# Optimization experiments

Measured on AMD Instinct MI355X. Metric: run time of the kernel, lower is better.

## Reference

```python
import jax, jax.numpy as jnp
import numpy as np

N_MLP = 16
LATENT = 1024
S0, S1, S2, OUT = 512, 256, 128, 3


def _make_grid(n_grid_step):
    # matches np.meshgrid (indexing='xy') then reshape(-1): points (x, y)
    p = np.linspace(-1.0, 1.0, n_grid_step, dtype=np.float32)
    X, Y = np.meshgrid(p, p)
    return jnp.asarray(np.stack([X.ravel(), Y.ravel()], axis=-1))  # [G, 2]


def setup_inputs() -> dict:
    key = jax.random.key(0)
    ks = jax.random.split(key, 12)
    sc = lambda fan_in: 1.0 / np.sqrt(fan_in)
    inp = {
        "x0": jax.random.normal(ks[0], (LATENT,), jnp.float32),
        "W0a": jax.random.normal(ks[1], (N_MLP, S0, LATENT), jnp.float32) * sc(LATENT),
        "b0a": jax.random.normal(ks[2], (N_MLP, S0), jnp.float32) * sc(LATENT),
        "W0b": jax.random.normal(ks[3], (N_MLP, S0, 2), jnp.float32) * sc(2),
        "b0b": jax.random.normal(ks[4], (N_MLP, S0), jnp.float32) * sc(2),
        "W1": jax.random.normal(ks[5], (N_MLP, S1, S0), jnp.float32) * sc(S0),
        "b1": jax.random.normal(ks[6], (N_MLP, S1), jnp.float32) * sc(S0),
        "W2": jax.random.normal(ks[7], (N_MLP, S2, S1), jnp.float32) * sc(S1),
        "b2": jax.random.normal(ks[8], (N_MLP, S2), jnp.float32) * sc(S1),
        "W3": jax.random.normal(ks[9], (N_MLP, OUT, S2), jnp.float32) * sc(S2),
        "b3": jax.random.normal(ks[10], (N_MLP, OUT), jnp.float32) * sc(S2),
        "n_grid_step": 128,
    }
    return inp


def reference(x0, W0a, b0a, W0b, b0b, W1, b1, W2, b2, W3, b3, n_grid_step):
    grid = _make_grid(n_grid_step)  # [G, 2], constant (requires_grad=False)
    # latent branch: [m, S0]
    y0_a = jnp.einsum('mol,l->mo', W0a, x0) + b0a
    # grid branch: [m, G, S0]
    y0_b = jnp.einsum('moi,gi->mgo', W0b, grid) + b0b[:, None, :]
    h = jax.nn.relu(y0_a[:, None, :] + y0_b)                        # [m,G,S0]
    h = jax.nn.relu(jnp.einsum('moh,mgh->mgo', W1, h) + b1[:, None, :])  # [m,G,S1]
    h = jax.nn.relu(jnp.einsum('moh,mgh->mgo', W2, h) + b2[:, None, :])  # [m,G,S2]
    out = jnp.tanh(jnp.einsum('moh,mgh->mgo', W3, h) + b3[:, None, :])   # [m,G,3]
    return out.reshape(-1, OUT)  # [m*G, 3]
```

## Files before the change

kernel.cpp:

```cpp
#include <hip/hip_runtime.h>
#include <hip/hip_bf16.h>
#include <cstdint>

typedef __bf16 bf16_t;
typedef bf16_t bf16x8 __attribute__((ext_vector_type(8)));
typedef float  f32x4  __attribute__((ext_vector_type(4)));

#define S0 512
#define S1 256
#define S2 128
#define NGRID 128
#define GPTS (NGRID*NGRID)
#define TG 64

#define WS_BASE 0u
#define WS_W1P  32768u
#define WS_W2P  (32768u + 4194304u)
#define WS_W3P  (32768u + 4194304u + 1048576u)

__global__ __launch_bounds__(256) void prep_base_k(
    const float* __restrict__ x0, const float* __restrict__ W0a,
    const float* __restrict__ b0a, const float* __restrict__ b0b,
    float* __restrict__ base)
{
  int wid = (blockIdx.x << 2) + (threadIdx.x >> 6);
  int L = threadIdx.x & 63;
  int m = wid >> 9, o = wid & 511;
  const float* wrow = W0a + ((size_t)(m*S0 + o) << 10);
  float acc = 0.f;
#pragma unroll
  for (int i = 0; i < 4; ++i) {
    f32x4 wv = *(const f32x4*)(wrow + i*256 + L*4);
    f32x4 xv = *(const f32x4*)(x0   + i*256 + L*4);
    acc += wv.x*xv.x + wv.y*xv.y + wv.z*xv.z + wv.w*xv.w;
  }
#pragma unroll
  for (int s = 32; s; s >>= 1) acc += __shfl_xor(acc, s, 64);
  if (L == 0) base[m*S0 + o] = acc + b0a[m*S0 + o] + b0b[m*S0 + o];
}

__global__ __launch_bounds__(256) void prep_pack_k(
    const float* __restrict__ W1, const float* __restrict__ W2,
    const float* __restrict__ W3, bf16_t* __restrict__ W1p,
    bf16_t* __restrict__ W2p, bf16_t* __restrict__ W3p)
{
  int T = blockIdx.x * 256 + threadIdx.x;
  const float* src = nullptr;
  bf16_t* dst = nullptr;
  if (T < 262144) {
    int L = T & 63, nt = (T >> 6) & 15, ks = (T >> 10) & 15, m = T >> 14;
    int n = nt*16 + (L & 15), k0 = ks*32 + ((L >> 4) & 3)*8;
    src = W1 + (size_t)(m*S1 + n)*S0 + k0;
    dst = W1p + (size_t)T*8;
  } else if (T < 262144 + 65536) {
    int T2 = T - 262144;
    int L = T2 & 63, nt = (T2 >> 6) & 7, ks = (T2 >> 9) & 7, m = T2 >> 12;
    int n = nt*16 + (L & 15), k0 = ks*32 + ((L >> 4) & 3)*8;
    src = W2 + (size_t)(m*S2 + n)*S1 + k0;
    dst = W2p + (size_t)T2*8;
  } else {
    int T3 = T - 327680;
    int L = T3 & 63, ks = (T3 >> 6) & 3, m = T3 >> 8;
    int n = L & 15, k0 = ks*32 + ((L >> 4) & 3)*8;
    dst = W3p + (size_t)T3*8;
    if (n < 3) src = W3 + (size_t)(m*3 + n)*S2 + k0;
  }
  bf16x8 v;
  if (src) {
    f32x4 a = *(const f32x4*)src;
    f32x4 b = *(const f32x4*)(src + 4);
    v[0]=(bf16_t)a.x; v[1]=(bf16_t)a.y; v[2]=(bf16_t)a.z; v[3]=(bf16_t)a.w;
    v[4]=(bf16_t)b.x; v[5]=(bf16_t)b.y; v[6]=(bf16_t)b.z; v[7]=(bf16_t)b.w;
  } else {
#pragma unroll
    for (int j = 0; j < 8; ++j) v[j] = (bf16_t)0.f;
  }
  *(bf16x8*)dst = v;
}

__global__ __launch_bounds__(256, 2) void fused_mlp_k(
    const float* __restrict__ base, const float* __restrict__ W0b,
    const bf16_t* __restrict__ W1p, const bf16_t* __restrict__ W2p,
    const bf16_t* __restrict__ W3p,
    const float* __restrict__ b1, const float* __restrict__ b2,
    const float* __restrict__ b3, float* __restrict__ out)
{
  __shared__ bf16_t sA1[TG*264];
  __shared__ bf16_t sA0[2][2048];

  const int bid  = blockIdx.x;
  const int m    = ((bid & 7) << 1) | (bid >> 11);
  const int tile = (bid >> 3) & 255;
  const int g0   = tile * TG;

  const int tid  = threadIdx.x;
  const int w    = tid >> 6, L = tid & 63;
  const int quad = L >> 4, lrow = L & 15;

  const float step = 2.0f / 127.0f;
  const float yv = -1.0f + (float)(tile >> 1) * step;
  const int   rc = (w << 4) | lrow;
  const float xv = -1.0f + (float)(((tile & 1) << 6) + rc) * step;

  const float* basep = base + m*S0;
  const float* w0bp  = W0b + (size_t)m*S0*2;

  f32x4 zero = {0.f, 0.f, 0.f, 0.f};
  f32x4 acc1[4][4];
#pragma unroll
  for (int a = 0; a < 4; ++a)
#pragma unroll
    for (int b = 0; b < 4; ++b) acc1[a][b] = zero;

  for (int ks = 0; ks < 16; ++ks) {
    int kk = ks*32 + quad*8;
    f32x4 cA = *(const f32x4*)(basep + kk);
    f32x4 cB = *(const f32x4*)(basep + kk + 4);
    f32x4 w0 = *(const f32x4*)(w0bp + kk*2);
    f32x4 w1v = *(const f32x4*)(w0bp + kk*2 + 4);
    f32x4 w2v = *(const f32x4*)(w0bp + kk*2 + 8);
    f32x4 w3v = *(const f32x4*)(w0bp + kk*2 + 12);
    float c[8]  = {cA.x, cA.y, cA.z, cA.w, cB.x, cB.y, cB.z, cB.w};
    float wx[8] = {w0.x, w0.z, w1v.x, w1v.z, w2v.x, w2v.z, w3v.x, w3v.z};
    float wy[8] = {w0.y, w0.w, w1v.y, w1v.w, w2v.y, w2v.w, w3v.y, w3v.w};
    bf16x8 hv;
#pragma unroll
    for (int j = 0; j < 8; ++j)
      hv[j] = (bf16_t)fmaxf(fmaf(wx[j], xv, fmaf(wy[j], yv, c[j])), 0.f);
    *(bf16x8*)(&sA0[ks & 1][tid * 8]) = hv;
    __syncthreads();

    bf16x8 af[4];
#pragma unroll
    for (int mt = 0; mt < 4; ++mt)
      af[mt] = *(const bf16x8*)(&sA0[ks & 1][(mt*64 + L)*8]);

    const bf16_t* bp = W1p + (((size_t)(m*16 + ks)*16 + w*4)*64 + L)*8;
#pragma unroll
    for (int n = 0; n < 4; ++n) {
      bf16x8 bfr = *(const bf16x8*)(bp + (size_t)n*512);
#pragma unroll
      for (int mt = 0; mt < 4; ++mt)
        acc1[mt][n] = __builtin_amdgcn_mfma_f32_16x16x32_bf16(af[mt], bfr, acc1[mt][n], 0, 0, 0);
    }
  }

#pragma unroll
  for (int n = 0; n < 4; ++n) {
    int col = (w*4 + n)*16 + lrow;
    float bb = b1[m*S1 + col];
#pragma unroll
    for (int mt = 0; mt < 4; ++mt)
#pragma unroll
      for (int p = 0; p < 4; ++p) {
        int row = mt*16 + quad*4 + p;
        sA1[row*264 + col] = (bf16_t)fmaxf(acc1[mt][n][p] + bb, 0.f);
      }
  }
  __syncthreads();

  f32x4 acc2[4][2];
#pragma unroll
  for (int a = 0; a < 4; ++a) { acc2[a][0] = zero; acc2[a][1] = zero; }
  for (int ks = 0; ks < 8; ++ks) {
    int k2 = ks*32 + quad*8;
    bf16x8 af[4];
#pragma unroll
    for (int mt = 0; mt < 4; ++mt)
      af[mt] = *(const bf16x8*)(&sA1[(mt*16 + lrow)*264 + k2]);
    const bf16_t* bp = W2p + (((size_t)(m*8 + ks)*8 + w*2)*64 + L)*8;
#pragma unroll
    for (int n = 0; n < 2; ++n) {
      bf16x8 bfr = *(const bf16x8*)(bp + (size_t)n*512);
#pragma unroll
      for (int mt = 0; mt < 4; ++mt)
        acc2[mt][n] = __builtin_amdgcn_mfma_f32_16x16x32_bf16(af[mt], bfr, acc2[mt][n], 0, 0, 0);
    }
  }
  __syncthreads();

  bf16_t* sH2 = sA1;
#pragma unroll
  for (int n = 0; n < 2; ++n) {
    int col = (w*2 + n)*16 + lrow;
    float bb = b2[m*S2 + col];
#pragma unroll
    for (int mt = 0; mt < 4; ++mt)
#pragma unroll
      for (int p = 0; p < 4; ++p) {
        int row = mt*16 + quad*4 + p;
        sH2[row*136 + col] = (bf16_t)fmaxf(acc2[mt][n][p] + bb, 0.f);
      }
  }
  __syncthreads();

  f32x4 acc3 = zero;
#pragma unroll
  for (int ks = 0; ks < 4; ++ks) {
    bf16x8 af = *(const bf16x8*)(&sH2[(w*16 + lrow)*136 + ks*32 + quad*8]);
    bf16x8 bfr = *(const bf16x8*)(W3p + (((size_t)m*4 + ks)*64 + L)*8);
    acc3 = __builtin_amdgcn_mfma_f32_16x16x32_bf16(af, bfr, acc3, 0, 0, 0);
  }
  if (lrow < 3) {
    float bb = b3[m*3 + lrow];
#pragma unroll
    for (int p = 0; p < 4; ++p) {
      int row = w*16 + quad*4 + p;
      out[((size_t)m*GPTS + g0 + row)*3 + lrow] = tanhf(acc3[p] + bb);
    }
  }
}

extern "C" void kernel_launch(void* const* d_in, const int* in_sizes, int n_in,
                              void* d_out, int out_size, void* d_ws, size_t ws_size,
                              hipStream_t stream) {
  const float* x0  = (const float*)d_in[0];
  const float* W0a = (const float*)d_in[1];
  const float* b0a = (const float*)d_in[2];
  const float* W0b = (const float*)d_in[3];
  const float* b0b = (const float*)d_in[4];
  const float* W1  = (const float*)d_in[5];
  const float* b1  = (const float*)d_in[6];
  const float* W2  = (const float*)d_in[7];
  const float* b2  = (const float*)d_in[8];
  const float* W3  = (const float*)d_in[9];
  const float* b3  = (const float*)d_in[10];

  char* ws = (char*)d_ws;
  float*  base = (float*)(ws + WS_BASE);
  bf16_t* W1p  = (bf16_t*)(ws + WS_W1P);
  bf16_t* W2p  = (bf16_t*)(ws + WS_W2P);
  bf16_t* W3p  = (bf16_t*)(ws + WS_W3P);
  float*  out  = (float*)d_out;

  prep_base_k<<<2048, 256, 0, stream>>>(x0, W0a, b0a, b0b, base);
  prep_pack_k<<<1296, 256, 0, stream>>>(W1, W2, W3, W1p, W2p, W3p);
  fused_mlp_k<<<4096, 256, 0, stream>>>(base, W0b, W1p, W2p, W3p, b1, b2, b3, out);
}
```

Before: 213.1 us.

## Compute layer-0 activations in registers, prefetch W1 fragments, merge prep kernels

Merges the two prep kernels into a single launch. The fused MLP kernel now builds the layer-0 activations directly in registers as MFMA operands, which removes the per-k-step shared-memory staging and its barrier. W1 fragments are prefetched one k-step ahead. Operands are swapped so the epilogues can write vectorized bf16x4 stores with a vector bias load, and tanhf is replaced by an exp2/rcp approximation. Occupancy is raised to 3 blocks per CU, and block-to-(m, tile) mapping is simplified, which may change L2 locality and register pressure.

After: 206.8 us. 2.9% less time.

```diff
diff --git a/kernel.cpp b/kernel.cpp
--- a/kernel.cpp
+++ b/kernel.cpp
@@ -4,6 +4,7 @@
 
 typedef __bf16 bf16_t;
 typedef bf16_t bf16x8 __attribute__((ext_vector_type(8)));
+typedef bf16_t bf16x4 __attribute__((ext_vector_type(4)));
 typedef float  f32x4  __attribute__((ext_vector_type(4)));
 
 #define S0 512
@@ -11,40 +12,43 @@
 #define S2 128
 #define NGRID 128
 #define GPTS (NGRID*NGRID)
-#define TG 64
 
 #define WS_BASE 0u
 #define WS_W1P  32768u
 #define WS_W2P  (32768u + 4194304u)
 #define WS_W3P  (32768u + 4194304u + 1048576u)
 
-__global__ __launch_bounds__(256) void prep_base_k(
+__device__ __forceinline__ float tanh_fast(float x) {
+  float e = __builtin_amdgcn_exp2f(x * 2.88539008f);
+  return fmaf(-2.0f, __builtin_amdgcn_rcpf(e + 1.0f), 1.0f);
+}
+
+__global__ __launch_bounds__(256) void prep_k(
     const float* __restrict__ x0, const float* __restrict__ W0a,
     const float* __restrict__ b0a, const float* __restrict__ b0b,
-    float* __restrict__ base)
+    const float* __restrict__ W1, const float* __restrict__ W2,
+    const float* __restrict__ W3, float* __restrict__ base,
+    bf16_t* __restrict__ W1p, bf16_t* __restrict__ W2p, bf16_t* __restrict__ W3p)
 {
-  int wid = (blockIdx.x << 2) + (threadIdx.x >> 6);
-  int L = threadIdx.x & 63;
-  int m = wid >> 9, o = wid & 511;
-  const float* wrow = W0a + ((size_t)(m*S0 + o) << 10);
-  float acc = 0.f;
-#pragma unroll
-  for (int i = 0; i < 4; ++i) {
-    f32x4 wv = *(const f32x4*)(wrow + i*256 + L*4);
-    f32x4 xv = *(const f32x4*)(x0   + i*256 + L*4);
-    acc += wv.x*xv.x + wv.y*xv.y + wv.z*xv.z + wv.w*xv.w;
-  }
-#pragma unroll
-  for (int s = 32; s; s >>= 1) acc += __shfl_xor(acc, s, 64);
-  if (L == 0) base[m*S0 + o] = acc + b0a[m*S0 + o] + b0b[m*S0 + o];
-}
-
-__global__ __launch_bounds__(256) void prep_pack_k(
-    const float* __restrict__ W1, const float* __restrict__ W2,
-    const float* __restrict__ W3, bf16_t* __restrict__ W1p,
-    bf16_t* __restrict__ W2p, bf16_t* __restrict__ W3p)
-{
-  int T = blockIdx.x * 256 + threadIdx.x;
+  if (blockIdx.x < 2048) {
+    int wid = (blockIdx.x << 2) + (threadIdx.x >> 6);
+    int L = threadIdx.x & 63;
+    int m = wid >> 9, o = wid & 511;
+    const float* wrow = W0a + ((size_t)(m*S0 + o) << 10);
+    float acc = 0.f;
+#pragma unroll
+    for (int i = 0; i < 4; ++i) {
+      f32x4 wv = *(const f32x4*)(wrow + i*256 + L*4);
+      f32x4 xv = *(const f32x4*)(x0   + i*256 + L*4);
+      acc += wv.x*xv.x + wv.y*xv.y + wv.z*xv.z + wv.w*xv.w;
+    }
+#pragma unroll
+    for (int s = 32; s; s >>= 1) acc += __shfl_xor(acc, s, 64);
+    if (L == 0) base[m*S0 + o] = acc + b0a[m*S0 + o] + b0b[m*S0 + o];
+    return;
+  }
+
+  int T = (blockIdx.x - 2048) * 256 + threadIdx.x;
   const float* src = nullptr;
   bf16_t* dst = nullptr;
   if (T < 262144) {
@@ -78,29 +82,27 @@
   *(bf16x8*)dst = v;
 }
 
-__global__ __launch_bounds__(256, 2) void fused_mlp_k(
+__global__ __launch_bounds__(256, 3) void fused_mlp_k(
     const float* __restrict__ base, const float* __restrict__ W0b,
     const bf16_t* __restrict__ W1p, const bf16_t* __restrict__ W2p,
     const bf16_t* __restrict__ W3p,
     const float* __restrict__ b1, const float* __restrict__ b2,
     const float* __restrict__ b3, float* __restrict__ out)
 {
-  __shared__ bf16_t sA1[TG*264];
-  __shared__ bf16_t sA0[2][2048];
+  __shared__ __align__(16) bf16_t sA1[64*264];
 
   const int bid  = blockIdx.x;
-  const int m    = ((bid & 7) << 1) | (bid >> 11);
-  const int tile = (bid >> 3) & 255;
-  const int g0   = tile * TG;
+  const int m    = bid >> 8;
+  const int tile = bid & 255;
+  const int g0   = tile * 64;
 
   const int tid  = threadIdx.x;
   const int w    = tid >> 6, L = tid & 63;
   const int quad = L >> 4, lrow = L & 15;
 
   const float step = 2.0f / 127.0f;
-  const float yv = -1.0f + (float)(tile >> 1) * step;
-  const int   rc = (w << 4) | lrow;
-  const float xv = -1.0f + (float)(((tile & 1) << 6) + rc) * step;
+  const float yv  = -1.0f + (float)(tile >> 1) * step;
+  const float xv0 = -1.0f + (float)(((tile & 1) << 6) + lrow) * step;
 
   const float* basep = base + m*S0;
   const float* w0bp  = W0b + (size_t)m*S0*2;
@@ -112,102 +114,122 @@
 #pragma unroll
     for (int b = 0; b < 4; ++b) acc1[a][b] = zero;
 
+  const bf16_t* bp1 = W1p + (((size_t)(m*16)*16 + w*4)*64 + L)*8;
+  bf16x8 Bc[4];
+#pragma unroll
+  for (int n = 0; n < 4; ++n) Bc[n] = *(const bf16x8*)(bp1 + (size_t)n*512);
+
+#pragma unroll 2
   for (int ks = 0; ks < 16; ++ks) {
-    int kk = ks*32 + quad*8;
-    f32x4 cA = *(const f32x4*)(basep + kk);
-    f32x4 cB = *(const f32x4*)(basep + kk + 4);
-    f32x4 w0 = *(const f32x4*)(w0bp + kk*2);
-    f32x4 w1v = *(const f32x4*)(w0bp + kk*2 + 4);
-    f32x4 w2v = *(const f32x4*)(w0bp + kk*2 + 8);
-    f32x4 w3v = *(const f32x4*)(w0bp + kk*2 + 12);
-    float c[8]  = {cA.x, cA.y, cA.z, cA.w, cB.x, cB.y, cB.z, cB.w};
-    float wx[8] = {w0.x, w0.z, w1v.x, w1v.z, w2v.x, w2v.z, w3v.x, w3v.z};
-    float wy[8] = {w0.y, w0.w, w1v.y, w1v.w, w2v.y, w2v.w, w3v.y, w3v.w};
-    bf16x8 hv;
-#pragma unroll
-    for (int j = 0; j < 8; ++j)
-      hv[j] = (bf16_t)fmaxf(fmaf(wx[j], xv, fmaf(wy[j], yv, c[j])), 0.f);
-    *(bf16x8*)(&sA0[ks & 1][tid * 8]) = hv;
-    __syncthreads();
-
-    bf16x8 af[4];
-#pragma unroll
-    for (int mt = 0; mt < 4; ++mt)
-      af[mt] = *(const bf16x8*)(&sA0[ks & 1][(mt*64 + L)*8]);
-
-    const bf16_t* bp = W1p + (((size_t)(m*16 + ks)*16 + w*4)*64 + L)*8;
-#pragma unroll
-    for (int n = 0; n < 4; ++n) {
-      bf16x8 bfr = *(const bf16x8*)(bp + (size_t)n*512);
-#pragma unroll
-      for (int mt = 0; mt < 4; ++mt)
-        acc1[mt][n] = __builtin_amdgcn_mfma_f32_16x16x32_bf16(af[mt], bfr, acc1[mt][n], 0, 0, 0);
-    }
-  }
-
-#pragma unroll
-  for (int n = 0; n < 4; ++n) {
-    int col = (w*4 + n)*16 + lrow;
-    float bb = b1[m*S1 + col];
-#pragma unroll
-    for (int mt = 0; mt < 4; ++mt)
-#pragma unroll
-      for (int p = 0; p < 4; ++p) {
-        int row = mt*16 + quad*4 + p;
-        sA1[row*264 + col] = (bf16_t)fmaxf(acc1[mt][n][p] + bb, 0.f);
-      }
+    const int kk = ks*32 + quad*8;
+    f32x4 cA  = *(const f32x4*)(basep + kk);
+    f32x4 cB  = *(const f32x4*)(basep + kk + 4);
+    f32x4 wv0 = *(const f32x4*)(w0bp + kk*2);
+    f32x4 wv1 = *(const f32x4*)(w0bp + kk*2 + 4);
+    f32x4 wv2 = *(const f32x4*)(w0bp + kk*2 + 8);
+    f32x4 wv3 = *(const f32x4*)(w0bp + kk*2 + 12);
+
+    bf16x8 Bn[4];
+    if (ks < 15) {
+#pragma unroll
+      for (int n = 0; n < 4; ++n)
+        Bn[n] = *(const bf16x8*)(bp1 + (size_t)(ks+1)*8192 + (size_t)n*512);
+    }
+
+    float t[8], wx[8];
+    t[0] = fmaf(wv0.y, yv, cA.x); wx[0] = wv0.x;
+    t[1] = fmaf(wv0.w, yv, cA.y); wx[1] = wv0.z;
+    t[2] = fmaf(wv1.y, yv, cA.z); wx[2] = wv1.x;
+    t[3] = fmaf(wv1.w, yv, cA.w); wx[3] = wv1.z;
+    t[4] = fmaf(wv2.y, yv, cB.x); wx[4] = wv2.x;
+    t[5] = fmaf(wv2.w, yv, cB.y); wx[5] = wv2.z;
+    t[6] = fmaf(wv3.y, yv, cB.z); wx[6] = wv3.x;
+    t[7] = fmaf(wv3.w, yv, cB.w); wx[7] = wv3.z;
+
+#pragma unroll
+    for (int mt = 0; mt < 4; ++mt) {
+      const float xr = xv0 + (float)(mt*16)*step;
+      bf16x8 af;
+#pragma unroll
+      for (int j = 0; j < 8; ++j)
+        af[j] = (bf16_t)fmaxf(fmaf(wx[j], xr, t[j]), 0.f);
+#pragma unroll
+      for (int n = 0; n < 4; ++n)
+        acc1[mt][n] = __builtin_amdgcn_mfma_f32_16x16x32_bf16(Bc[n], af, acc1[mt][n], 0, 0, 0);
+    }
+    if (ks < 15) {
+#pragma unroll
+      for (int n = 0; n < 4; ++n) Bc[n] = Bn[n];
+    }
+  }
+
+#pragma unroll
+  for (int nb = 0; nb < 4; ++nb) {
+    const int col = w*64 + nb*16 + quad*4;
+    f32x4 bb = *(const f32x4*)(b1 + m*S1 + col);
+#pragma unroll
+    for (int mt = 0; mt < 4; ++mt) {
+      const int row = mt*16 + lrow;
+      bf16x4 v;
+#pragma unroll
+      for (int p = 0; p < 4; ++p)
+        v[p] = (bf16_t)fmaxf(acc1[mt][nb][p] + bb[p], 0.f);
+      *(bf16x4*)(&sA1[row*264 + col]) = v;
+    }
   }
   __syncthreads();
 
   f32x4 acc2[4][2];
 #pragma unroll
   for (int a = 0; a < 4; ++a) { acc2[a][0] = zero; acc2[a][1] = zero; }
+  const bf16_t* bp2 = W2p + (((size_t)(m*8)*8 + w*2)*64 + L)*8;
+#pragma unroll 2
   for (int ks = 0; ks < 8; ++ks) {
-    int k2 = ks*32 + quad*8;
+    const int k2 = ks*32 + quad*8;
     bf16x8 af[4];
 #pragma unroll
     for (int mt = 0; mt < 4; ++mt)
       af[mt] = *(const bf16x8*)(&sA1[(mt*16 + lrow)*264 + k2]);
-    const bf16_t* bp = W2p + (((size_t)(m*8 + ks)*8 + w*2)*64 + L)*8;
-#pragma unroll
-    for (int n = 0; n < 2; ++n) {
-      bf16x8 bfr = *(const bf16x8*)(bp + (size_t)n*512);
-#pragma unroll
-      for (int mt = 0; mt < 4; ++mt)
-        acc2[mt][n] = __builtin_amdgcn_mfma_f32_16x16x32_bf16(af[mt], bfr, acc2[mt][n], 0, 0, 0);
-    }
+    bf16x8 b0f = *(const bf16x8*)(bp2 + (size_t)ks*4096);
+    bf16x8 b1f = *(const bf16x8*)(bp2 + (size_t)ks*4096 + 512);
+#pragma unroll
+    for (int mt = 0; mt < 4; ++mt)
+      acc2[mt][0] = __builtin_amdgcn_mfma_f32_16x16x32_bf16(b0f, af[mt], acc2[mt][0], 0, 0, 0);
+#pragma unroll
+    for (int mt = 0; mt < 4; ++mt)
+      acc2[mt][1] = __builtin_amdgcn_mfma_f32_16x16x32_bf16(b1f, af[mt], acc2[mt][1], 0, 0, 0);
   }
   __syncthreads();
 
   bf16_t* sH2 = sA1;
 #pragma unroll
-  for (int n = 0; n < 2; ++n) {
-    int col = (w*2 + n)*16 + lrow;
-    float bb = b2[m*S2 + col];
-#pragma unroll
-    for (int mt = 0; mt < 4; ++mt)
-#pragma unroll
-      for (int p = 0; p < 4; ++p) {
-        int row = mt*16 + quad*4 + p;
-        sH2[row*136 + col] = (bf16_t)fmaxf(acc2[mt][n][p] + bb, 0.f);
-      }
+  for (int nb = 0; nb < 2; ++nb) {
+    const int col = w*32 + nb*16 + quad*4;
+    f32x4 bb = *(const f32x4*)(b2 + m*S2 + col);
+#pragma unroll
+    for (int mt = 0; mt < 4; ++mt) {
+      const int row = mt*16 + lrow;
+      bf16x4 v;
+#pragma unroll
+      for (int p = 0; p < 4; ++p)
+        v[p] = (bf16_t)fmaxf(acc2[mt][nb][p] + bb[p], 0.f);
+      *(bf16x4*)(&sH2[row*136 + col]) = v;
+    }
   }
   __syncthreads();
 
   f32x4 acc3 = zero;
 #pragma unroll
   for (int ks = 0; ks < 4; ++ks) {
-    bf16x8 af = *(const bf16x8*)(&sH2[(w*16 + lrow)*136 + ks*32 + quad*8]);
+    bf16x8 af  = *(const bf16x8*)(&sH2[(w*16 + lrow)*136 + ks*32 + quad*8]);
     bf16x8 bfr = *(const bf16x8*)(W3p + (((size_t)m*4 + ks)*64 + L)*8);
-    acc3 = __builtin_amdgcn_mfma_f32_16x16x32_bf16(af, bfr, acc3, 0, 0, 0);
-  }
-  if (lrow < 3) {
-    float bb = b3[m*3 + lrow];
-#pragma unroll
-    for (int p = 0; p < 4; ++p) {
-      int row = w*16 + quad*4 + p;
-      out[((size_t)m*GPTS + g0 + row)*3 + lrow] = tanhf(acc3[p] + bb);
-    }
+    acc3 = __builtin_amdgcn_mfma_f32_16x16x32_bf16(bfr, af, acc3, 0, 0, 0);
+  }
+  if (quad == 0) {
+    const size_t o = ((size_t)m*GPTS + g0 + w*16 + lrow)*3;
+    out[o + 0] = tanh_fast(acc3[0] + b3[m*3 + 0]);
+    out[o + 1] = tanh_fast(acc3[1] + b3[m*3 + 1]);
+    out[o + 2] = tanh_fast(acc3[2] + b3[m*3 + 2]);
   }
 }
 
@@ -233,7 +255,6 @@
   bf16_t* W3p  = (bf16_t*)(ws + WS_W3P);
   float*  out  = (float*)d_out;
 
-  prep_base_k<<<2048, 256, 0, stream>>>(x0, W0a, b0a, b0b, base);
-  prep_pack_k<<<1296, 256, 0, stream>>>(W1, W2, W3, W1p, W2p, W3p);
+  prep_k<<<3344, 256, 0, stream>>>(x0, W0a, b0a, b0b, W1, W2, W3, base, W1p, W2p, W3p);
   fused_mlp_k<<<4096, 256, 0, stream>>>(base, W0b, W1p, W2p, W3p, b1, b2, b3, out);
 }
```
